# Performance work log

Measured on AMD Instinct MI355X. Metric: run time of the kernel, lower is better.

The kernel has to match this reference:

```python
import jax, jax.numpy as jnp
import numpy as np

N = 50000   # nodes
E = 200000  # edges
C = 32      # conv_dim
ND = 75     # n_atom_features
ED = 12     # n_bond_features
L = 3       # num_layer
G = 500     # num graphs in batch
HID = 5     # neurons_message
EPS = 1e-5


def leaky(v):
    return jnp.where(v > 0, v, 0.01 * v)


def setup_inputs() -> dict:
    key = jax.random.key(0)
    ks = jax.random.split(key, 16)
    x = jax.random.normal(ks[0], (N, ND), jnp.float32)
    edge_index = jax.random.randint(ks[1], (2, E), 0, N, jnp.int32)
    edge_attr = jax.random.uniform(ks[2], (E, ED), jnp.float32)
    batch = jnp.sort(jax.random.randint(ks[3], (N,), 0, G, jnp.int32))
    return {
        "x": x,
        "edge_index": edge_index,
        "edge_attr": edge_attr,
        "batch": batch,
        "lin_W": jax.random.normal(ks[4], (ND, C), jnp.float32) * 0.1,
        "lin_b": jnp.zeros((C,), jnp.float32),
        "mes_W1": jax.random.normal(ks[5], (L, ED, HID), jnp.float32) * 0.3,
        "mes_b1": jnp.zeros((L, HID), jnp.float32),
        "mes_W2": jax.random.normal(ks[6], (L, HID, C * C), jnp.float32) * 0.05,
        "mes_b2": jnp.zeros((L, C * C), jnp.float32),
        "root_W": jax.random.normal(ks[7], (L, C, C), jnp.float32) * 0.1,
        "conv_b": jnp.zeros((L, C), jnp.float32),
        "bn_g": jnp.ones((L, C), jnp.float32),
        "bn_b": jnp.zeros((L, C), jnp.float32),
        "pred_W": jax.random.normal(ks[8], (C, 1), jnp.float32) * 0.1,
        "pred_b": jnp.zeros((1,), jnp.float32),
    }


def reference(x, edge_index, edge_attr, batch, lin_W, lin_b, mes_W1, mes_b1,
              mes_W2, mes_b2, root_W, conv_b, bn_g, bn_b, pred_W, pred_b):
    src, dst = edge_index[0], edge_index[1]
    # initial atom projection
    h = leaky(x @ lin_W + lin_b)  # [N, C]
    for l in range(L):
        # edge MLP -> per-edge weight matrix [E, C, C]
        w = jnp.maximum(edge_attr @ mes_W1[l] + mes_b1[l], 0.0)
        w = (w @ mes_W2[l] + mes_b2[l]).reshape(E, C, C)
        # gather source features, per-edge matmul, scatter-add to targets
        msg = jnp.einsum('ec,ecd->ed', h[src], w)  # [E, C]
        agg = jax.ops.segment_sum(msg, dst, num_segments=N)  # [N, C]
        out = agg + h @ root_W[l] + conv_b[l]
        # batch norm (batch statistics over nodes)
        mu = out.mean(axis=0)
        var = out.var(axis=0)
        out = (out - mu) / jnp.sqrt(var + EPS) * bn_g[l] + bn_b[l]
        if l < L - 1:
            out = leaky(out)
        h = out  # JK == 'last'
    # graph readout: scatter_add over batch ids, then prediction head
    g = jax.ops.segment_sum(h, batch, num_segments=G)  # [G, C]
    return g @ pred_W + pred_b  # [G, 1]
```

## Files before the change

### kernel.cpp

```cpp
#include <hip/hip_runtime.h>

namespace {

constexpr int kN  = 50000;
constexpr int kE  = 200000;
constexpr int kC  = 32;
constexpr int kND = 75;
constexpr int kED = 12;
constexpr int kL  = 3;
constexpr int kG  = 500;
constexpr int kH  = 5;
constexpr float kEps = 1e-5f;

__device__ __forceinline__ unsigned bf16rn(float x) {
    unsigned u = __float_as_uint(x);
    return (u + 0x7FFFu + ((u >> 16) & 1u)) >> 16;
}
__device__ __forceinline__ float bf16lo(unsigned p) { return __uint_as_float(p << 16); }
__device__ __forceinline__ float bf16hi(unsigned p) { return __uint_as_float(p & 0xFFFF0000u); }

__global__ __launch_bounds__(256) void init_h(
    const float* __restrict__ x, const float* __restrict__ W,
    const float* __restrict__ b, float* __restrict__ h)
{
    __shared__ float sW[kND * kC];
    __shared__ float sb[kC];
    int t = threadIdx.x;
    for (int i = t; i < kND * kC; i += 256) sW[i] = W[i];
    if (t < kC) sb[t] = b[t];
    __syncthreads();
    int c = t & 31;
    int n = blockIdx.x * 8 + (t >> 5);
    if (n >= kN) return;
    const float* xr = x + n * kND;
    float acc = sb[c];
    #pragma unroll 5
    for (int f = 0; f < kND; ++f) acc = fmaf(xr[f], sW[f * kC + c], acc);
    h[n * kC + c] = acc > 0.f ? acc : 0.01f * acc;
}

__global__ __launch_bounds__(256) void y_root(
    const float* __restrict__ h,
    const float* __restrict__ W2,
    const float* __restrict__ b2,
    const float* __restrict__ rootW,
    const float* __restrict__ convb,
    unsigned short* __restrict__ Y, float* __restrict__ obuf,
    float* __restrict__ stats)
{
    __shared__ float sM[7 * 1024];
    __shared__ float sh[32 * kC];
    __shared__ float scb[kC];
    int t = threadIdx.x;
    if (blockIdx.x == 0 && t < 64) stats[t] = 0.f;
    for (int i = t; i < 5 * 1024; i += 256) sM[i] = W2[i];
    for (int i = t; i < 1024; i += 256) {
        sM[5 * 1024 + i] = b2[i];
        sM[6 * 1024 + i] = rootW[i];
    }
    if (t < kC) scb[t] = convb[t];

    int base = blockIdx.x * 32;
    #pragma unroll
    for (int j = 0; j < 4; ++j) {
        int idx = t + j * 256;
        int n = base + (idx >> 5);
        sh[idx] = (n < kN) ? h[n * kC + (idx & 31)] : 0.f;
    }
    __syncthreads();

    int d = t & 31;
    int li = t >> 5;
    float acc[7][4];
    #pragma unroll
    for (int k = 0; k < 7; ++k)
        #pragma unroll
        for (int j = 0; j < 4; ++j) acc[k][j] = 0.f;

    #pragma unroll 4
    for (int c = 0; c < kC; ++c) {
        int off = c * 32 + d;
        float m0 = sM[0 * 1024 + off];
        float m1 = sM[1 * 1024 + off];
        float m2 = sM[2 * 1024 + off];
        float m3 = sM[3 * 1024 + off];
        float m4 = sM[4 * 1024 + off];
        float m5 = sM[5 * 1024 + off];
        float m6 = sM[6 * 1024 + off];
        #pragma unroll
        for (int j = 0; j < 4; ++j) {
            float hc = sh[(li * 4 + j) * kC + c];
            acc[0][j] = fmaf(hc, m0, acc[0][j]);
            acc[1][j] = fmaf(hc, m1, acc[1][j]);
            acc[2][j] = fmaf(hc, m2, acc[2][j]);
            acc[3][j] = fmaf(hc, m3, acc[3][j]);
            acc[4][j] = fmaf(hc, m4, acc[4][j]);
            acc[5][j] = fmaf(hc, m5, acc[5][j]);
            acc[6][j] = fmaf(hc, m6, acc[6][j]);
        }
    }
    #pragma unroll
    for (int j = 0; j < 4; ++j) {
        int n = base + li * 4 + j;
        if (n >= kN) continue;
        unsigned* yr = (unsigned*)(Y + (size_t)n * 192 + d * 6);
        yr[0] = bf16rn(acc[0][j]) | (bf16rn(acc[1][j]) << 16);
        yr[1] = bf16rn(acc[2][j]) | (bf16rn(acc[3][j]) << 16);
        yr[2] = bf16rn(acc[4][j]) | (bf16rn(acc[5][j]) << 16);
        obuf[n * kC + d] = acc[6][j] + scb[d];
    }
}

__global__ __launch_bounds__(256) void edge_msg(
    const int* __restrict__ ei_src, const int* __restrict__ ei_dst,
    const float* __restrict__ ea,
    const float* __restrict__ W1, const float* __restrict__ b1,
    const unsigned short* __restrict__ Y, float* __restrict__ obuf)
{
    __shared__ float sW1[kED * kH];
    __shared__ float sb1[kH];
    int t = threadIdx.x;
    if (t < kED * kH) sW1[t] = W1[t];
    if (t < kH) sb1[t] = b1[t];
    __syncthreads();
    int gid = blockIdx.x * 256 + t;
    int e = gid >> 5;
    int d = gid & 31;
    if (e >= kE) return;
    int src = ei_src[e];
    int dst = ei_dst[e];
    float hv = 0.f;
    if (d < kH) {
        const float* er = ea + e * kED;
        float a = sb1[d];
        #pragma unroll
        for (int j = 0; j < kED; ++j) a = fmaf(er[j], sW1[j * kH + d], a);
        hv = a > 0.f ? a : 0.f;
    }
    float h0 = __shfl(hv, 0, 32);
    float h1 = __shfl(hv, 1, 32);
    float h2 = __shfl(hv, 2, 32);
    float h3 = __shfl(hv, 3, 32);
    float h4 = __shfl(hv, 4, 32);
    const unsigned* yr = (const unsigned*)(Y + (size_t)src * 192 + d * 6);
    unsigned p0 = yr[0];
    unsigned p1 = yr[1];
    unsigned p2 = yr[2];
    float m = bf16hi(p2);
    m = fmaf(h0, bf16lo(p0), m);
    m = fmaf(h1, bf16hi(p0), m);
    m = fmaf(h2, bf16lo(p1), m);
    m = fmaf(h3, bf16hi(p1), m);
    m = fmaf(h4, bf16lo(p2), m);
    atomicAdd(&obuf[dst * kC + d], m);
}

__global__ __launch_bounds__(256) void bn_reduce(
    const float* __restrict__ obuf, float* __restrict__ stats)
{
    __shared__ float ls[256];
    __shared__ float lq[256];
    int t = threadIdx.x;
    int c = t & 31;
    int row = t >> 5;
    float s = 0.f, q = 0.f;
    for (int n = blockIdx.x * 8 + row; n < kN; n += gridDim.x * 8) {
        float v = obuf[n * kC + c];
        s += v; q += v * v;
    }
    ls[t] = s; lq[t] = q;
    __syncthreads();
    if (t < 128) { ls[t] += ls[t + 128]; lq[t] += lq[t + 128]; }
    __syncthreads();
    if (t < 64) { ls[t] += ls[t + 64]; lq[t] += lq[t + 64]; }
    __syncthreads();
    if (t < 32) {
        atomicAdd(&stats[t], ls[t] + ls[t + 32]);
        atomicAdd(&stats[32 + t], lq[t] + lq[t + 32]);
    }
}

__global__ __launch_bounds__(256) void bn_norm_mid(
    const float* __restrict__ obuf, const float* __restrict__ stats,
    const float* __restrict__ g, const float* __restrict__ b,
    float* __restrict__ h)
{
    int idx = blockIdx.x * 256 + threadIdx.x;
    if (idx >= kN * kC) return;
    int c = idx & 31;
    float mu = stats[c] * (1.f / kN);
    float var = stats[32 + c] * (1.f / kN) - mu * mu;
    float inv = rsqrtf(var + kEps);
    float v = (obuf[idx] - mu) * inv * g[c] + b[c];
    h[idx] = v > 0.f ? v : 0.01f * v;
}

__global__ __launch_bounds__(256) void bn_norm_final(
    const float* __restrict__ obuf, const float* __restrict__ stats,
    const float* __restrict__ g, const float* __restrict__ b,
    float* __restrict__ vbuf,
    const float* __restrict__ predW,
    float* __restrict__ out, const float* __restrict__ pred_b)
{
    int idx = blockIdx.x * 256 + threadIdx.x;
    if (idx < kG) out[idx] = pred_b[0];
    if (idx >= kN * kC) return;
    int c = idx & 31;
    float mu = stats[c] * (1.f / kN);
    float var = stats[32 + c] * (1.f / kN) - mu * mu;
    float inv = rsqrtf(var + kEps);
    float v = (obuf[idx] - mu) * inv * g[c] + b[c];
    float pv = v * predW[c];
    #pragma unroll
    for (int off = 16; off > 0; off >>= 1) pv += __shfl_down(pv, off, 32);
    if (c == 0) vbuf[idx >> 5] = pv;
}

__global__ __launch_bounds__(256) void seg_readout(
    const float* __restrict__ vbuf, const int* __restrict__ batch,
    float* __restrict__ out)
{
    __shared__ float ls[kG];
    int t = threadIdx.x;
    for (int i = t; i < kG; i += 256) ls[i] = 0.f;
    __syncthreads();
    int base = blockIdx.x * 2048 + t * 8;
    int cur = -1;
    float acc = 0.f;
    #pragma unroll
    for (int i = 0; i < 8; ++i) {
        int n = base + i;
        if (n >= kN) break;
        int gidx = batch[n];
        float val = vbuf[n];
        if (gidx != cur) {
            if (cur >= 0) atomicAdd(&ls[cur], acc);
            cur = gidx;
            acc = val;
        } else {
            acc += val;
        }
    }
    if (cur >= 0) atomicAdd(&ls[cur], acc);
    __syncthreads();
    for (int gidx = t; gidx < kG; gidx += 256) {
        float s = ls[gidx];
        if (s != 0.f) atomicAdd(&out[gidx], s);
    }
}

}

extern "C" void kernel_launch(void* const* d_in, const int* in_sizes, int n_in,
                              void* d_out, int out_size, void* d_ws, size_t ws_size,
                              hipStream_t stream)
{
    const float* x      = (const float*)d_in[0];
    const int*   ei     = (const int*)d_in[1];
    const float* ea     = (const float*)d_in[2];
    const int*   batch  = (const int*)d_in[3];
    const float* lin_W  = (const float*)d_in[4];
    const float* lin_b  = (const float*)d_in[5];
    const float* mes_W1 = (const float*)d_in[6];
    const float* mes_b1 = (const float*)d_in[7];
    const float* mes_W2 = (const float*)d_in[8];
    const float* mes_b2 = (const float*)d_in[9];
    const float* root_W = (const float*)d_in[10];
    const float* conv_b = (const float*)d_in[11];
    const float* bn_g   = (const float*)d_in[12];
    const float* bn_b   = (const float*)d_in[13];
    const float* pred_W = (const float*)d_in[14];
    const float* pred_b = (const float*)d_in[15];
    float* out = (float*)d_out;

    float* hbuf  = (float*)d_ws;
    float* obuf  = hbuf + (size_t)kN * kC;
    unsigned short* Y = (unsigned short*)(obuf + (size_t)kN * kC);
    float* stats = (float*)(Y + (size_t)kN * 192);
    float* vbuf  = (float*)Y;

    init_h<<<(kN + 7) / 8, 256, 0, stream>>>(x, lin_W, lin_b, hbuf);

    int nb = (kN * kC + 255) / 256;
    for (int l = 0; l < kL; ++l) {
        y_root<<<(kN + 31) / 32, 256, 0, stream>>>(
            hbuf, mes_W2 + l * kH * kC * kC, mes_b2 + l * kC * kC,
            root_W + l * kC * kC, conv_b + l * kC, Y, obuf, stats);
        edge_msg<<<(kE * 32 + 255) / 256, 256, 0, stream>>>(
            ei, ei + kE, ea, mes_W1 + l * kED * kH, mes_b1 + l * kH, Y, obuf);
        bn_reduce<<<512, 256, 0, stream>>>(obuf, stats);
        if (l < kL - 1)
            bn_norm_mid<<<nb, 256, 0, stream>>>(
                obuf, stats, bn_g + l * kC, bn_b + l * kC, hbuf);
        else
            bn_norm_final<<<nb, 256, 0, stream>>>(
                obuf, stats, bn_g + l * kC, bn_b + l * kC, vbuf,
                pred_W, out, pred_b);
    }

    seg_readout<<<(kN + 2047) / 2048, 256, 0, stream>>>(vbuf, batch, out);
}
```

Measured before the change: 340.7 us.

## Use MFMA bf16 for projections, precompute edge hidden, fuse BN into y_root

Replaces the scalar FMA node projection and per-layer Y/root computation with MFMA 16x16x32 bf16 instructions and stores h in bf16. Edge hidden-layer activations for all three layers are precomputed once in a separate kernel, so edge_msg no longer recomputes the small edge MLP. The mid-layer batch-norm kernel is folded into the next y_root load, and the stats reset moves into edge_msg. It also pads the Y rows to 16-byte vector loads. The cost is lower precision (bf16 inputs and weights) and extra workspace for the packed hidden values.

```diff
diff --git a/kernel.cpp b/kernel.cpp
--- a/kernel.cpp
+++ b/kernel.cpp
@@ -2,157 +2,198 @@
 
 namespace {
 
-constexpr int kN  = 50000;
-constexpr int kE  = 200000;
-constexpr int kC  = 32;
-constexpr int kND = 75;
-constexpr int kED = 12;
-constexpr int kL  = 3;
-constexpr int kG  = 500;
-constexpr int kH  = 5;
+constexpr int kN = 50000, kE = 200000, kG = 500;
 constexpr float kEps = 1e-5f;
 
-__device__ __forceinline__ unsigned bf16rn(float x) {
+typedef short v8s __attribute__((ext_vector_type(8)));
+typedef float v4f __attribute__((ext_vector_type(4)));
+
+__device__ __forceinline__ unsigned short bf16rn(float x) {
     unsigned u = __float_as_uint(x);
-    return (u + 0x7FFFu + ((u >> 16) & 1u)) >> 16;
+    return (unsigned short)((u + 0x7FFFu + ((u >> 16) & 1u)) >> 16);
 }
 __device__ __forceinline__ float bf16lo(unsigned p) { return __uint_as_float(p << 16); }
 __device__ __forceinline__ float bf16hi(unsigned p) { return __uint_as_float(p & 0xFFFF0000u); }
-
-__global__ __launch_bounds__(256) void init_h(
+__device__ __forceinline__ unsigned pk2(float a, float b) {
+    return (unsigned)bf16rn(a) | ((unsigned)bf16rn(b) << 16);
+}
+
+__global__ __launch_bounds__(1024) void init_h(
     const float* __restrict__ x, const float* __restrict__ W,
-    const float* __restrict__ b, float* __restrict__ h)
-{
-    __shared__ float sW[kND * kC];
-    __shared__ float sb[kC];
-    int t = threadIdx.x;
-    for (int i = t; i < kND * kC; i += 256) sW[i] = W[i];
-    if (t < kC) sb[t] = b[t];
-    __syncthreads();
-    int c = t & 31;
-    int n = blockIdx.x * 8 + (t >> 5);
-    if (n >= kN) return;
-    const float* xr = x + n * kND;
-    float acc = sb[c];
-    #pragma unroll 5
-    for (int f = 0; f < kND; ++f) acc = fmaf(xr[f], sW[f * kC + c], acc);
-    h[n * kC + c] = acc > 0.f ? acc : 0.01f * acc;
-}
-
-__global__ __launch_bounds__(256) void y_root(
-    const float* __restrict__ h,
-    const float* __restrict__ W2,
-    const float* __restrict__ b2,
-    const float* __restrict__ rootW,
-    const float* __restrict__ convb,
-    unsigned short* __restrict__ Y, float* __restrict__ obuf,
+    const float* __restrict__ b, unsigned short* __restrict__ h16)
+{
+    __shared__ unsigned short sx[256 * 96];
+    __shared__ unsigned short sW[32 * 96];
+    int t = threadIdx.x;
+    for (int i = t; i < 256 * 96; i += 1024) sx[i] = 0;
+    for (int i = t; i < 32 * 96; i += 1024) sW[i] = 0;
+    __syncthreads();
+    int tb = blockIdx.x * 256;
+    int cnt = min(256, kN - tb);
+    for (int i = t; i < cnt * 75; i += 1024) {
+        int n = i / 75, f = i - n * 75;
+        sx[n * 96 + f] = bf16rn(x[(size_t)tb * 75 + i]);
+    }
+    for (int i = t; i < 75 * 32; i += 1024) {
+        int f = i >> 5, c = i & 31;
+        sW[c * 96 + f] = bf16rn(W[i]);
+    }
+    __syncthreads();
+    int l15 = t & 15, quad = (t >> 4) & 3, w = t >> 6;
+    int n = tb + w * 16 + l15;
+    unsigned* H = (unsigned*)h16;
+    #pragma unroll
+    for (int tile = 0; tile < 2; ++tile) {
+        v4f acc = {0.f, 0.f, 0.f, 0.f};
+        #pragma unroll
+        for (int kc = 0; kc < 3; ++kc) {
+            v8s a  = *(const v8s*)&sW[(tile * 16 + l15) * 96 + kc * 32 + quad * 8];
+            v8s bb = *(const v8s*)&sx[(w * 16 + l15) * 96 + kc * 32 + quad * 8];
+            acc = __builtin_amdgcn_mfma_f32_16x16x32_bf16(a, bb, acc, 0, 0, 0);
+        }
+        if (n < kN) {
+            int c0 = tile * 16 + quad * 4;
+            float v0 = acc[0] + b[c0],     v1 = acc[1] + b[c0 + 1];
+            float v2 = acc[2] + b[c0 + 2], v3 = acc[3] + b[c0 + 3];
+            v0 = v0 > 0.f ? v0 : 0.01f * v0;  v1 = v1 > 0.f ? v1 : 0.01f * v1;
+            v2 = v2 > 0.f ? v2 : 0.01f * v2;  v3 = v3 > 0.f ? v3 : 0.01f * v3;
+            H[n * 16 + (c0 >> 1)]     = pk2(v0, v1);
+            H[n * 16 + (c0 >> 1) + 1] = pk2(v2, v3);
+        }
+    }
+}
+
+__global__ __launch_bounds__(256) void hid_pre(
+    const float* __restrict__ ea, const float* __restrict__ W1,
+    const float* __restrict__ b1, unsigned* __restrict__ hidpk)
+{
+    __shared__ float sE[256 * 13];
+    __shared__ float sW[195];
+    int t = threadIdx.x;
+    for (int i = t; i < 195; i += 256) sW[i] = (i < 180) ? W1[i] : b1[i - 180];
+    int base = blockIdx.x * 256;
+    int cnt = min(256, kE - base);
+    for (int i = t; i < cnt * 12; i += 256) {
+        int el = i / 12, f = i - el * 12;
+        sE[el * 13 + f] = ea[(size_t)base * 12 + i];
+    }
+    __syncthreads();
+    if (t >= cnt) return;
+    int e = base + t;
+    float ef[12];
+    #pragma unroll
+    for (int j = 0; j < 12; ++j) ef[j] = sE[t * 13 + j];
+    #pragma unroll
+    for (int l = 0; l < 3; ++l) {
+        float h[5];
+        #pragma unroll
+        for (int k = 0; k < 5; ++k) h[k] = sW[180 + l * 5 + k];
+        #pragma unroll
+        for (int f = 0; f < 12; ++f)
+            #pragma unroll
+            for (int k = 0; k < 5; ++k)
+                h[k] = fmaf(ef[f], sW[l * 60 + f * 5 + k], h[k]);
+        #pragma unroll
+        for (int k = 0; k < 5; ++k) h[k] = h[k] > 0.f ? h[k] : 0.f;
+        size_t o = ((size_t)l * kE + e) * 3;
+        hidpk[o + 0] = pk2(h[0], h[1]);
+        hidpk[o + 1] = pk2(h[2], h[3]);
+        hidpk[o + 2] = pk2(h[4], 0.f);
+    }
+}
+
+__global__ __launch_bounds__(1024) void y_root(
+    const unsigned short* __restrict__ h16, float* __restrict__ obuf,
+    const float* __restrict__ W2, const float* __restrict__ b2,
+    const float* __restrict__ rW, const float* __restrict__ convb,
+    const float* __restrict__ stats,
+    const float* __restrict__ gPrev, const float* __restrict__ bPrev,
+    int first, unsigned short* __restrict__ Yus)
+{
+    __shared__ unsigned short sh[256 * 32];
+    __shared__ unsigned short sB[256 * 32];
+    int t = threadIdx.x;
+    int tb = blockIdx.x * 256;
+    int cnt = min(256, kN - tb);
+    for (int i = t; i < 8192; i += 1024) {
+        int co = i >> 5, c = i & 31, d = co >> 3, k = co & 7;
+        float v = (k < 5) ? W2[k * 1024 + c * 32 + d]
+                : (k == 5) ? b2[c * 32 + d]
+                : (k == 6) ? rW[c * 32 + d] : 0.f;
+        sB[co * 32 + c] = bf16rn(v);
+    }
+    if (first) {
+        #pragma unroll
+        for (int j = 0; j < 8; ++j) {
+            int idx = t + j * 1024;
+            int nl = idx >> 5, c = idx & 31;
+            sh[idx] = (nl < cnt) ? h16[(size_t)(tb + nl) * 32 + c] : (unsigned short)0;
+        }
+    } else {
+        int c = t & 31;
+        float mu = stats[c] * (1.f / kN);
+        float var = stats[32 + c] * (1.f / kN) - mu * mu;
+        float ivg = rsqrtf(var + kEps) * gPrev[c];
+        float bb = bPrev[c];
+        #pragma unroll
+        for (int j = 0; j < 8; ++j) {
+            int idx = t + j * 1024;
+            int nl = idx >> 5;
+            float v = 0.f;
+            if (nl < cnt) {
+                float o = obuf[(size_t)(tb + nl) * 32 + c];
+                v = (o - mu) * ivg + bb;
+                v = v > 0.f ? v : 0.01f * v;
+            }
+            sh[idx] = bf16rn(v);
+        }
+    }
+    __syncthreads();
+    int l15 = t & 15, quad = (t >> 4) & 3, w = t >> 6;
+    int n = tb + w * 16 + l15;
+    v8s bn_ = *(const v8s*)&sh[(w * 16 + l15) * 32 + quad * 8];
+    unsigned* Ydw = (unsigned*)Yus;
+    #pragma unroll
+    for (int i = 0; i < 16; ++i) {
+        v8s a = *(const v8s*)&sB[(i * 16 + l15) * 32 + quad * 8];
+        v4f acc = {0.f, 0.f, 0.f, 0.f};
+        acc = __builtin_amdgcn_mfma_f32_16x16x32_bf16(a, bn_, acc, 0, 0, 0);
+        if (n < kN) {
+            int cb = i * 16 + quad * 4;
+            int d = cb >> 3, koff = cb & 7;
+            if (koff == 0) {
+                Ydw[(size_t)n * 128 + d * 4]     = pk2(acc[0], acc[1]);
+                Ydw[(size_t)n * 128 + d * 4 + 1] = pk2(acc[2], acc[3]);
+            } else {
+                Ydw[(size_t)n * 128 + d * 4 + 2] = pk2(acc[0], acc[1]);
+                obuf[(size_t)n * 32 + d] = acc[2] + convb[d];
+            }
+        }
+    }
+}
+
+__global__ __launch_bounds__(256) void edge_msg(
+    const int* __restrict__ ei, const unsigned* __restrict__ hp,
+    const unsigned short* __restrict__ Yus, float* __restrict__ obuf,
     float* __restrict__ stats)
 {
-    __shared__ float sM[7 * 1024];
-    __shared__ float sh[32 * kC];
-    __shared__ float scb[kC];
     int t = threadIdx.x;
     if (blockIdx.x == 0 && t < 64) stats[t] = 0.f;
-    for (int i = t; i < 5 * 1024; i += 256) sM[i] = W2[i];
-    for (int i = t; i < 1024; i += 256) {
-        sM[5 * 1024 + i] = b2[i];
-        sM[6 * 1024 + i] = rootW[i];
-    }
-    if (t < kC) scb[t] = convb[t];
-
-    int base = blockIdx.x * 32;
-    #pragma unroll
-    for (int j = 0; j < 4; ++j) {
-        int idx = t + j * 256;
-        int n = base + (idx >> 5);
-        sh[idx] = (n < kN) ? h[n * kC + (idx & 31)] : 0.f;
-    }
-    __syncthreads();
-
-    int d = t & 31;
-    int li = t >> 5;
-    float acc[7][4];
-    #pragma unroll
-    for (int k = 0; k < 7; ++k)
-        #pragma unroll
-        for (int j = 0; j < 4; ++j) acc[k][j] = 0.f;
-
-    #pragma unroll 4
-    for (int c = 0; c < kC; ++c) {
-        int off = c * 32 + d;
-        float m0 = sM[0 * 1024 + off];
-        float m1 = sM[1 * 1024 + off];
-        float m2 = sM[2 * 1024 + off];
-        float m3 = sM[3 * 1024 + off];
-        float m4 = sM[4 * 1024 + off];
-        float m5 = sM[5 * 1024 + off];
-        float m6 = sM[6 * 1024 + off];
-        #pragma unroll
-        for (int j = 0; j < 4; ++j) {
-            float hc = sh[(li * 4 + j) * kC + c];
-            acc[0][j] = fmaf(hc, m0, acc[0][j]);
-            acc[1][j] = fmaf(hc, m1, acc[1][j]);
-            acc[2][j] = fmaf(hc, m2, acc[2][j]);
-            acc[3][j] = fmaf(hc, m3, acc[3][j]);
-            acc[4][j] = fmaf(hc, m4, acc[4][j]);
-            acc[5][j] = fmaf(hc, m5, acc[5][j]);
-            acc[6][j] = fmaf(hc, m6, acc[6][j]);
-        }
-    }
-    #pragma unroll
-    for (int j = 0; j < 4; ++j) {
-        int n = base + li * 4 + j;
-        if (n >= kN) continue;
-        unsigned* yr = (unsigned*)(Y + (size_t)n * 192 + d * 6);
-        yr[0] = bf16rn(acc[0][j]) | (bf16rn(acc[1][j]) << 16);
-        yr[1] = bf16rn(acc[2][j]) | (bf16rn(acc[3][j]) << 16);
-        yr[2] = bf16rn(acc[4][j]) | (bf16rn(acc[5][j]) << 16);
-        obuf[n * kC + d] = acc[6][j] + scb[d];
-    }
-}
-
-__global__ __launch_bounds__(256) void edge_msg(
-    const int* __restrict__ ei_src, const int* __restrict__ ei_dst,
-    const float* __restrict__ ea,
-    const float* __restrict__ W1, const float* __restrict__ b1,
-    const unsigned short* __restrict__ Y, float* __restrict__ obuf)
-{
-    __shared__ float sW1[kED * kH];
-    __shared__ float sb1[kH];
-    int t = threadIdx.x;
-    if (t < kED * kH) sW1[t] = W1[t];
-    if (t < kH) sb1[t] = b1[t];
-    __syncthreads();
     int gid = blockIdx.x * 256 + t;
-    int e = gid >> 5;
-    int d = gid & 31;
-    if (e >= kE) return;
-    int src = ei_src[e];
-    int dst = ei_dst[e];
-    float hv = 0.f;
-    if (d < kH) {
-        const float* er = ea + e * kED;
-        float a = sb1[d];
-        #pragma unroll
-        for (int j = 0; j < kED; ++j) a = fmaf(er[j], sW1[j * kH + d], a);
-        hv = a > 0.f ? a : 0.f;
-    }
-    float h0 = __shfl(hv, 0, 32);
-    float h1 = __shfl(hv, 1, 32);
-    float h2 = __shfl(hv, 2, 32);
-    float h3 = __shfl(hv, 3, 32);
-    float h4 = __shfl(hv, 4, 32);
-    const unsigned* yr = (const unsigned*)(Y + (size_t)src * 192 + d * 6);
-    unsigned p0 = yr[0];
-    unsigned p1 = yr[1];
-    unsigned p2 = yr[2];
-    float m = bf16hi(p2);
-    m = fmaf(h0, bf16lo(p0), m);
-    m = fmaf(h1, bf16hi(p0), m);
-    m = fmaf(h2, bf16lo(p1), m);
-    m = fmaf(h3, bf16hi(p1), m);
-    m = fmaf(h4, bf16lo(p2), m);
-    atomicAdd(&obuf[dst * kC + d], m);
+    int e = gid >> 5, d = gid & 31;
+    int src = ei[e];
+    int dst = ei[kE + e];
+    unsigned q0 = hp[(size_t)e * 3 + 0];
+    unsigned q1 = hp[(size_t)e * 3 + 1];
+    unsigned q2 = hp[(size_t)e * 3 + 2];
+    uint4 p = *(const uint4*)(Yus + (size_t)src * 256 + d * 8);
+    float m = bf16hi(p.z);
+    m = fmaf(bf16lo(q0), bf16lo(p.x), m);
+    m = fmaf(bf16hi(q0), bf16hi(p.x), m);
+    m = fmaf(bf16lo(q1), bf16lo(p.y), m);
+    m = fmaf(bf16hi(q1), bf16hi(p.y), m);
+    m = fmaf(bf16lo(q2), bf16lo(p.z), m);
+    atomicAdd(&obuf[(size_t)dst * 32 + d], m);
 }
 
 __global__ __launch_bounds__(256) void bn_reduce(
@@ -161,11 +202,10 @@
     __shared__ float ls[256];
     __shared__ float lq[256];
     int t = threadIdx.x;
-    int c = t & 31;
-    int row = t >> 5;
+    int c = t & 31, row = t >> 5;
     float s = 0.f, q = 0.f;
     for (int n = blockIdx.x * 8 + row; n < kN; n += gridDim.x * 8) {
-        float v = obuf[n * kC + c];
+        float v = obuf[(size_t)n * 32 + c];
         s += v; q += v * v;
     }
     ls[t] = s; lq[t] = q;
@@ -180,31 +220,15 @@
     }
 }
 
-__global__ __launch_bounds__(256) void bn_norm_mid(
-    const float* __restrict__ obuf, const float* __restrict__ stats,
-    const float* __restrict__ g, const float* __restrict__ b,
-    float* __restrict__ h)
-{
-    int idx = blockIdx.x * 256 + threadIdx.x;
-    if (idx >= kN * kC) return;
-    int c = idx & 31;
-    float mu = stats[c] * (1.f / kN);
-    float var = stats[32 + c] * (1.f / kN) - mu * mu;
-    float inv = rsqrtf(var + kEps);
-    float v = (obuf[idx] - mu) * inv * g[c] + b[c];
-    h[idx] = v > 0.f ? v : 0.01f * v;
-}
-
 __global__ __launch_bounds__(256) void bn_norm_final(
     const float* __restrict__ obuf, const float* __restrict__ stats,
     const float* __restrict__ g, const float* __restrict__ b,
-    float* __restrict__ vbuf,
-    const float* __restrict__ predW,
+    float* __restrict__ vbuf, const float* __restrict__ predW,
     float* __restrict__ out, const float* __restrict__ pred_b)
 {
     int idx = blockIdx.x * 256 + threadIdx.x;
     if (idx < kG) out[idx] = pred_b[0];
-    if (idx >= kN * kC) return;
+    if (idx >= kN * 32) return;
     int c = idx & 31;
     float mu = stats[c] * (1.f / kN);
     float var = stats[32 + c] * (1.f / kN) - mu * mu;
@@ -225,27 +249,23 @@
     for (int i = t; i < kG; i += 256) ls[i] = 0.f;
     __syncthreads();
     int base = blockIdx.x * 2048 + t * 8;
-    int cur = -1;
-    float acc = 0.f;
+    int cur = -1; float acc = 0.f;
     #pragma unroll
     for (int i = 0; i < 8; ++i) {
         int n = base + i;
         if (n >= kN) break;
-        int gidx = batch[n];
+        int gi = batch[n];
         float val = vbuf[n];
-        if (gidx != cur) {
+        if (gi != cur) {
             if (cur >= 0) atomicAdd(&ls[cur], acc);
-            cur = gidx;
-            acc = val;
-        } else {
-            acc += val;
-        }
+            cur = gi; acc = val;
+        } else acc += val;
     }
     if (cur >= 0) atomicAdd(&ls[cur], acc);
     __syncthreads();
-    for (int gidx = t; gidx < kG; gidx += 256) {
-        float s = ls[gidx];
-        if (s != 0.f) atomicAdd(&out[gidx], s);
+    for (int i = t; i < kG; i += 256) {
+        float s = ls[i];
+        if (s != 0.f) atomicAdd(&out[i], s);
     }
 }
 
@@ -273,30 +293,29 @@
     const float* pred_b = (const float*)d_in[15];
     float* out = (float*)d_out;
 
-    float* hbuf  = (float*)d_ws;
-    float* obuf  = hbuf + (size_t)kN * kC;
-    unsigned short* Y = (unsigned short*)(obuf + (size_t)kN * kC);
-    float* stats = (float*)(Y + (size_t)kN * 192);
-    float* vbuf  = (float*)Y;
-
-    init_h<<<(kN + 7) / 8, 256, 0, stream>>>(x, lin_W, lin_b, hbuf);
-
-    int nb = (kN * kC + 255) / 256;
-    for (int l = 0; l < kL; ++l) {
-        y_root<<<(kN + 31) / 32, 256, 0, stream>>>(
-            hbuf, mes_W2 + l * kH * kC * kC, mes_b2 + l * kC * kC,
-            root_W + l * kC * kC, conv_b + l * kC, Y, obuf, stats);
-        edge_msg<<<(kE * 32 + 255) / 256, 256, 0, stream>>>(
-            ei, ei + kE, ea, mes_W1 + l * kED * kH, mes_b1 + l * kH, Y, obuf);
+    char* wsb = (char*)d_ws;
+    float* stats = (float*)wsb;
+    unsigned short* h16 = (unsigned short*)(wsb + 256);
+    float* obuf = (float*)(h16 + (size_t)kN * 32);
+    unsigned short* Yus = (unsigned short*)(obuf + (size_t)kN * 32);
+    unsigned* hidpk = (unsigned*)(Yus + (size_t)kN * 256);
+    float* vbuf = (float*)Yus;
+
+    init_h<<<(kN + 255) / 256, 1024, 0, stream>>>(x, lin_W, lin_b, h16);
+    hid_pre<<<(kE + 255) / 256, 256, 0, stream>>>(ea, mes_W1, mes_b1, hidpk);
+
+    for (int l = 0; l < 3; ++l) {
+        y_root<<<(kN + 255) / 256, 1024, 0, stream>>>(
+            h16, obuf, mes_W2 + (size_t)l * 5120, mes_b2 + (size_t)l * 1024,
+            root_W + (size_t)l * 1024, conv_b + l * 32, stats,
+            bn_g + (l ? (l - 1) * 32 : 0), bn_b + (l ? (l - 1) * 32 : 0),
+            l == 0 ? 1 : 0, Yus);
+        edge_msg<<<kE * 32 / 256, 256, 0, stream>>>(
+            ei, hidpk + (size_t)l * kE * 3, Yus, obuf, stats);
         bn_reduce<<<512, 256, 0, stream>>>(obuf, stats);
-        if (l < kL - 1)
-            bn_norm_mid<<<nb, 256, 0, stream>>>(
-                obuf, stats, bn_g + l * kC, bn_b + l * kC, hbuf);
-        else
-            bn_norm_final<<<nb, 256, 0, stream>>>(
-                obuf, stats, bn_g + l * kC, bn_b + l * kC, vbuf,
-                pred_W, out, pred_b);
-    }
-
+    }
+
+    bn_norm_final<<<(kN * 32 + 255) / 256, 256, 0, stream>>>(
+        obuf, stats, bn_g + 64, bn_b + 64, vbuf, pred_W, out, pred_b);
     seg_readout<<<(kN + 2047) / 2048, 256, 0, stream>>>(vbuf, batch, out);
 }
```

Measured after the change: 310.2 us. 8.9% less time.
